# Optimization experiments

Measured on AMD Instinct MI355X. Metric: run time of the kernel, lower is better.

The kernel has to match this reference:

```python
import jax, jax.numpy as jnp
import numpy as np
import math

D_INNER = 1024
D_STATE = 16
DT_RANK = 64  # d_inner // 16


def setup_inputs() -> dict:
    key = jax.random.key(0)
    ks = jax.random.split(key, 8)
    B, L, M, D, R = 2, 2048, D_INNER, D_STATE, DT_RANK
    x = jax.random.normal(ks[0], (B, L, M), dtype=jnp.float32)
    z = jax.random.normal(ks[1], (B, L, M), dtype=jnp.float32)
    # Parameters (torch Linear weight layout: [out, in])
    x_proj_w = jax.random.normal(ks[2], (R + 2 * D, M), dtype=jnp.float32) / jnp.sqrt(M)
    dt_init_std = R ** (-0.5)
    dt_proj_w = jax.random.uniform(ks[3], (M, R), dtype=jnp.float32, minval=-dt_init_std, maxval=dt_init_std)
    dt_min, dt_max = 0.001, 0.1
    dt = jnp.exp(jax.random.uniform(ks[4], (M,), dtype=jnp.float32) * (math.log(dt_max) - math.log(dt_min)) + math.log(dt_min))
    dt_proj_b = dt + jnp.log(-jnp.expm1(-dt))  # inverse softplus init
    A_log = jax.random.normal(ks[5], (D, M), dtype=jnp.float32) * 0.1
    D_param = jnp.ones((M,), dtype=jnp.float32)
    return {"x": x, "z": z, "x_proj_w": x_proj_w, "dt_proj_w": dt_proj_w,
            "dt_proj_b": dt_proj_b, "A_log": A_log, "D_param": D_param}


def reference(x, z, x_proj_w, dt_proj_w, dt_proj_b, A_log, D_param):
    B, L, M = x.shape
    D = A_log.shape[0]
    R = dt_proj_w.shape[1]
    # Input-dependent projections
    xp = jnp.einsum('blm,nm->bln', x, x_proj_w)          # [B,L,R+2D]
    dt_in = xp[..., :R]
    B_ssm = xp[..., R:R + D]                              # [B,L,D]
    C_ssm = xp[..., R + D:]                               # [B,L,D]
    dt = jax.nn.softplus(jnp.einsum('blr,mr->blm', dt_in, dt_proj_w) + dt_proj_b)  # [B,L,M]
    A = -jnp.exp(A_log).T                                 # [M,D]

    def step(h, inp):
        dt_t, x_t, B_t, C_t = inp                         # [B,M],[B,M],[B,D],[B,D]
        dA = jnp.exp(dt_t[:, :, None] * A[None])          # [B,M,D]
        h = dA * h + (dt_t * x_t)[:, :, None] * B_t[:, None, :]
        y_t = jnp.einsum('bmd,bd->bm', h, C_t) + D_param * x_t
        return h, y_t

    h0 = jnp.zeros((B, M, D), dtype=x.dtype)
    xs = (jnp.swapaxes(dt, 0, 1), jnp.swapaxes(x, 0, 1),
          jnp.swapaxes(B_ssm, 0, 1), jnp.swapaxes(C_ssm, 0, 1))
    _, ys = jax.lax.scan(step, h0, xs)                    # ys: [L,B,M]
    y = jnp.swapaxes(ys, 0, 1)
    y = y * jax.nn.silu(z)
    return y
```

## Files before the change

kernel.cpp:

```cpp
#include <hip/hip_runtime.h>
#include <math.h>

#define BB 2
#define LL 2048
#define MM 1024
#define DD 16
#define RR 64
#define NN 96
#define BLROWS (BB*LL)
#define NCH 64
#define CLEN (LL/NCH)

#define OFF_XP    0
#define OFF_DT    (OFF_XP + BLROWS*NN)
#define OFF_A2    (OFF_DT + BLROWS*MM/2)
#define OFF_HEND  (OFF_A2 + MM*DD)
#define OFF_DTSUM (OFF_HEND + NCH*BB*MM*DD)

typedef __attribute__((ext_vector_type(8))) short bf16x8;
typedef __attribute__((ext_vector_type(4))) float f32x4;
typedef __attribute__((ext_vector_type(4))) unsigned short u16x4;

union BF8 { bf16x8 v; unsigned u[4]; };

__device__ __forceinline__ unsigned cvtpk(float a, float b) {
  unsigned r;
  asm("v_cvt_pk_bf16_f32 %0, %1, %2" : "=v"(r) : "v"(a), "v"(b));
  return r;
}

__device__ __forceinline__ float softplusf(float v) {
  return v > 20.f ? v : __logf(1.f + __expf(v));
}

__device__ __forceinline__ short f2bf(float f) {
  union { float f; unsigned u; } v; v.f = f;
  unsigned r = v.u + 0x7FFFu + ((v.u >> 16) & 1u);
  return (short)(r >> 16);
}

__device__ __forceinline__ float bf2f(unsigned short u) {
  return __uint_as_float((unsigned)u << 16);
}

__device__ __forceinline__ float dpp_xor1(float v) {
  int i = __builtin_amdgcn_mov_dpp(__float_as_int(v), 0xB1, 0xF, 0xF, true);
  return __int_as_float(i);
}
__device__ __forceinline__ float dpp_xor2(float v) {
  int i = __builtin_amdgcn_mov_dpp(__float_as_int(v), 0x4E, 0xF, 0xF, true);
  return __int_as_float(i);
}

#define XP_GEMM_BLOCKS ((BLROWS/16)*3)
__global__ __launch_bounds__(64) void k_xp(const float* __restrict__ x,
                                           const float* __restrict__ W,
                                           const float* __restrict__ A_log,
                                           float* __restrict__ ws) {
  if (blockIdx.x >= XP_GEMM_BLOCKS) {
    int idx = (blockIdx.x - XP_GEMM_BLOCKS) * 64 + threadIdx.x;
    int m = idx >> 4, d = idx & 15;
    ws[OFF_A2 + idx] = -__expf(A_log[d * MM + m]);
    return;
  }
  float* xp = ws + OFF_XP;
  int lane = threadIdx.x;
  int rt = blockIdx.x / 3, np = blockIdx.x % 3;
  int lr = lane & 15, lk = lane >> 4;
  const float* xr = x + (size_t)(rt * 16 + lr) * MM + lk * 8;
  const float* wr0 = W + (size_t)(np * 32 + lr) * MM + lk * 8;
  const float* wr1 = W + (size_t)(np * 32 + 16 + lr) * MM + lk * 8;
  f32x4 acc0 = {0.f, 0.f, 0.f, 0.f}, acc1 = {0.f, 0.f, 0.f, 0.f};
#pragma unroll 2
  for (int kk = 0; kk < MM; kk += 32) {
    float4 xa = *(const float4*)(xr + kk);
    float4 xb = *(const float4*)(xr + kk + 4);
    float4 p0 = *(const float4*)(wr0 + kk);
    float4 p1 = *(const float4*)(wr0 + kk + 4);
    float4 q0 = *(const float4*)(wr1 + kk);
    float4 q1 = *(const float4*)(wr1 + kk + 4);
    BF8 a, b0, b1;
    a.u[0] = cvtpk(xa.x, xa.y); a.u[1] = cvtpk(xa.z, xa.w);
    a.u[2] = cvtpk(xb.x, xb.y); a.u[3] = cvtpk(xb.z, xb.w);
    b0.u[0] = cvtpk(p0.x, p0.y); b0.u[1] = cvtpk(p0.z, p0.w);
    b0.u[2] = cvtpk(p1.x, p1.y); b0.u[3] = cvtpk(p1.z, p1.w);
    b1.u[0] = cvtpk(q0.x, q0.y); b1.u[1] = cvtpk(q0.z, q0.w);
    b1.u[2] = cvtpk(q1.x, q1.y); b1.u[3] = cvtpk(q1.z, q1.w);
    acc0 = __builtin_amdgcn_mfma_f32_16x16x32_bf16(a.v, b0.v, acc0, 0, 0, 0);
    acc1 = __builtin_amdgcn_mfma_f32_16x16x32_bf16(a.v, b1.v, acc1, 0, 0, 0);
  }
  int r0 = rt * 16 + lk * 4, c0 = np * 32 + lr;
#pragma unroll
  for (int e = 0; e < 4; ++e) {
    xp[(size_t)(r0 + e) * NN + c0] = acc0[e];
    xp[(size_t)(r0 + e) * NN + c0 + 16] = acc1[e];
  }
}

__global__ __launch_bounds__(64) void k_dt(const float* __restrict__ dtW,
                                           const float* __restrict__ dtb,
                                           float* __restrict__ ws) {
  const float* xp = ws + OFF_XP;
  unsigned short* dt16 = (unsigned short*)(ws + OFF_DT);
  int lane = threadIdx.x;
  int rt = blockIdx.x >> 3, mg = blockIdx.x & 7;
  int lr = lane & 15, lk = lane >> 4;
  const float* xr = xp + (size_t)(rt * 16 + lr) * NN + lk * 8;
  BF8 a0, a1;
  {
    float4 xa = *(const float4*)(xr);
    float4 xb = *(const float4*)(xr + 4);
    float4 xc = *(const float4*)(xr + 32);
    float4 xd = *(const float4*)(xr + 36);
    a0.u[0] = cvtpk(xa.x, xa.y); a0.u[1] = cvtpk(xa.z, xa.w);
    a0.u[2] = cvtpk(xb.x, xb.y); a0.u[3] = cvtpk(xb.z, xb.w);
    a1.u[0] = cvtpk(xc.x, xc.y); a1.u[1] = cvtpk(xc.z, xc.w);
    a1.u[2] = cvtpk(xd.x, xd.y); a1.u[3] = cvtpk(xd.z, xd.w);
  }
  int r0 = rt * 16 + lk * 4;
#pragma unroll 2
  for (int mt = 0; mt < 8; ++mt) {
    int mcol = (mg * 8 + mt) * 16 + lr;
    const float* wr = dtW + (size_t)mcol * RR + lk * 8;
    float4 p0 = *(const float4*)(wr);
    float4 p1 = *(const float4*)(wr + 4);
    float4 p2 = *(const float4*)(wr + 32);
    float4 p3 = *(const float4*)(wr + 36);
    BF8 b0, b1;
    b0.u[0] = cvtpk(p0.x, p0.y); b0.u[1] = cvtpk(p0.z, p0.w);
    b0.u[2] = cvtpk(p1.x, p1.y); b0.u[3] = cvtpk(p1.z, p1.w);
    b1.u[0] = cvtpk(p2.x, p2.y); b1.u[1] = cvtpk(p2.z, p2.w);
    b1.u[2] = cvtpk(p3.x, p3.y); b1.u[3] = cvtpk(p3.z, p3.w);
    f32x4 acc = {0.f, 0.f, 0.f, 0.f};
    acc = __builtin_amdgcn_mfma_f32_16x16x32_bf16(a0.v, b0.v, acc, 0, 0, 0);
    acc = __builtin_amdgcn_mfma_f32_16x16x32_bf16(a1.v, b1.v, acc, 0, 0, 0);
    float bv = dtb[mcol];
#pragma unroll
    for (int e = 0; e < 4; ++e)
      dt16[(size_t)(r0 + e) * MM + mcol] = (unsigned short)f2bf(softplusf(acc[e] + bv));
  }
}

__global__ __launch_bounds__(256) void k_scan1(const float* __restrict__ x,
                                               float* __restrict__ ws) {
  const float* xp = ws + OFF_XP;
  const float* A2t = ws + OFF_A2;
  float* hend = ws + OFF_HEND;
  float* dtsum = ws + OFF_DTSUM;
  __shared__ __align__(16) float ds_[CLEN * 64];
  __shared__ __align__(16) float xs_[CLEN * 64];
  __shared__ __align__(16) float bs[CLEN * DD];
  int wg = blockIdx.x;
  int mw = wg & 15, c = (wg >> 4) & (NCH - 1), b = wg >> 10;
  int t = threadIdx.x;
  int ml = t >> 2, dsub = t & 3;
  int m0 = mw * 64, m = m0 + ml;
  int l0 = c * CLEN;
  const unsigned short* dtg = (const unsigned short*)(ws + OFF_DT) + (size_t)(b * LL + l0) * MM + m0;
  const float* xg = x + (size_t)(b * LL + l0) * MM + m0;
#pragma unroll
  for (int i = t; i < CLEN * 16; i += 256) {
    int lo = i >> 4, q = i & 15;
    u16x4 dv = *(const u16x4*)&dtg[(size_t)lo * MM + q * 4];
    *(float4*)&ds_[lo * 64 + q * 4] = make_float4(bf2f(dv[0]), bf2f(dv[1]), bf2f(dv[2]), bf2f(dv[3]));
    *(float4*)&xs_[lo * 64 + q * 4] = *(const float4*)&xg[(size_t)lo * MM + q * 4];
  }
  for (int i = t; i < CLEN * DD; i += 256) {
    int r = i >> 4, cc = i & 15;
    bs[i] = xp[(size_t)(b * LL + l0 + r) * NN + RR + cc];
  }
  __syncthreads();
  float4 A2v = *(const float4*)&A2t[m * DD + dsub * 4];
  float h0_ = 0.f, h1_ = 0.f, h2_ = 0.f, h3_ = 0.f, S = 0.f;
#pragma unroll 4
  for (int lo = 0; lo < CLEN; ++lo) {
    float dtv = ds_[lo * 64 + ml];
    float xv = xs_[lo * 64 + ml];
    float4 Bv = *(const float4*)&bs[lo * DD + dsub * 4];
    S += dtv;
    float dtx = dtv * xv;
    h0_ = __expf(dtv * A2v.x) * h0_ + dtx * Bv.x;
    h1_ = __expf(dtv * A2v.y) * h1_ + dtx * Bv.y;
    h2_ = __expf(dtv * A2v.z) * h2_ + dtx * Bv.z;
    h3_ = __expf(dtv * A2v.w) * h3_ + dtx * Bv.w;
  }
  size_t o = ((size_t)((c * BB + b) * MM + m)) * DD + dsub * 4;
  *(float4*)&hend[o] = make_float4(h0_, h1_, h2_, h3_);
  if (dsub == 0) dtsum[(c * BB + b) * MM + m] = S;
}

__global__ __launch_bounds__(256) void k_scan2(float* __restrict__ ws) {
  int t = blockIdx.x * 256 + threadIdx.x;
  int d = t & 15, m = (t >> 4) & 1023, b = t >> 14;
  float* hend = ws + OFF_HEND;
  const float* dtsum = ws + OFF_DTSUM;
  float A2 = ws[OFF_A2 + m * DD + d];
  const size_t hstride = (size_t)BB * MM * DD;
  const int sstride = BB * MM;
  size_t o = ((size_t)b * MM + m) * DD + d;
  int si = b * MM + m;
  float h = 0.f;
  float he = hend[o], S = dtsum[si];
  for (int c = 0; c < NCH; ++c) {
    float heN = 0.f, SN = 0.f;
    if (c + 1 < NCH) {
      heN = hend[o + hstride];
      SN = dtsum[si + sstride];
    }
    hend[o] = h;
    h = __expf(A2 * S) * h + he;
    he = heN; S = SN;
    o += hstride; si += sstride;
  }
}

__global__ __launch_bounds__(256) void k_scan3(const float* __restrict__ x,
                                               const float* __restrict__ z,
                                               const float* __restrict__ Dp,
                                               float* __restrict__ out,
                                               float* __restrict__ ws) {
  const float* xp = ws + OFF_XP;
  const float* A2t = ws + OFF_A2;
  const float* h0w = ws + OFF_HEND;
  __shared__ __align__(16) float ds_[CLEN * 64];
  __shared__ __align__(16) float xs_[CLEN * 64];
  __shared__ __align__(16) float zs_[CLEN * 64];
  __shared__ __align__(16) float bs[CLEN * 32];
  int wg = blockIdx.x;
  int mw = wg & 15, c = (wg >> 4) & (NCH - 1), b = wg >> 10;
  int t = threadIdx.x;
  int ml = t >> 2, dsub = t & 3;
  int m0 = mw * 64, m = m0 + ml;
  int l0 = c * CLEN;
  const unsigned short* dtg = (const unsigned short*)(ws + OFF_DT) + (size_t)(b * LL + l0) * MM + m0;
  const float* xg = x + (size_t)(b * LL + l0) * MM + m0;
  const float* zg = z + (size_t)(b * LL + l0) * MM + m0;
#pragma unroll
  for (int i = t; i < CLEN * 16; i += 256) {
    int lo = i >> 4, q = i & 15;
    u16x4 dv = *(const u16x4*)&dtg[(size_t)lo * MM + q * 4];
    *(float4*)&ds_[lo * 64 + q * 4] = make_float4(bf2f(dv[0]), bf2f(dv[1]), bf2f(dv[2]), bf2f(dv[3]));
    *(float4*)&xs_[lo * 64 + q * 4] = *(const float4*)&xg[(size_t)lo * MM + q * 4];
    *(float4*)&zs_[lo * 64 + q * 4] = *(const float4*)&zg[(size_t)lo * MM + q * 4];
  }
  for (int i = t; i < CLEN * 32; i += 256) {
    int r = i >> 5, cc = i & 31;
    bs[i] = xp[(size_t)(b * LL + l0 + r) * NN + RR + cc];
  }
  __syncthreads();
  float4 A2v = *(const float4*)&A2t[m * DD + dsub * 4];
  size_t o = ((size_t)((c * BB + b) * MM + m)) * DD + dsub * 4;
  float4 hv = *(const float4*)&h0w[o];
  float h0_ = hv.x, h1_ = hv.y, h2_ = hv.z, h3_ = hv.w;
  float Dpm = Dp[m];
  size_t idx = ((size_t)(b * LL + l0)) * MM + m;
#pragma unroll 4
  for (int lo = 0; lo < CLEN; ++lo) {
    float dtv = ds_[lo * 64 + ml];
    float xv = xs_[lo * 64 + ml];
    float zv = zs_[lo * 64 + ml];
    float4 Bv = *(const float4*)&bs[lo * 32 + dsub * 4];
    float4 Cv = *(const float4*)&bs[lo * 32 + DD + dsub * 4];
    float dtx = dtv * xv;
    h0_ = __expf(dtv * A2v.x) * h0_ + dtx * Bv.x;
    h1_ = __expf(dtv * A2v.y) * h1_ + dtx * Bv.y;
    h2_ = __expf(dtv * A2v.z) * h2_ + dtx * Bv.z;
    h3_ = __expf(dtv * A2v.w) * h3_ + dtx * Bv.w;
    float yp = h0_ * Cv.x + h1_ * Cv.y + h2_ * Cv.z + h3_ * Cv.w;
    yp += dpp_xor1(yp);
    yp += dpp_xor2(yp);
    float sig = __builtin_amdgcn_rcpf(1.f + __expf(-zv));
    if (dsub == 0)
      out[idx + (size_t)lo * MM] = (yp + Dpm * xv) * zv * sig;
  }
}

extern "C" void kernel_launch(void* const* d_in, const int* in_sizes, int n_in,
                              void* d_out, int out_size, void* d_ws, size_t ws_size,
                              hipStream_t stream) {
  const float* x = (const float*)d_in[0];
  const float* z = (const float*)d_in[1];
  const float* W = (const float*)d_in[2];
  const float* dtW = (const float*)d_in[3];
  const float* dtb = (const float*)d_in[4];
  const float* A_log = (const float*)d_in[5];
  const float* Dp = (const float*)d_in[6];
  float* out = (float*)d_out;
  float* ws = (float*)d_ws;

  k_xp<<<XP_GEMM_BLOCKS + (MM * DD / 64), 64, 0, stream>>>(x, W, A_log, ws);
  k_dt<<<(BLROWS / 16) * 8, 64, 0, stream>>>(dtW, dtb, ws);
  k_scan1<<<16 * NCH * BB, 256, 0, stream>>>(x, ws);
  k_scan2<<<128, 256, 0, stream>>>(ws);
  k_scan3<<<16 * NCH * BB, 256, 0, stream>>>(x, z, Dp, out, ws);
}
```

Measured before the change: 85.96 us.

## Split-K xp GEMM across four waves, widen dt grid, store scan inputs as bf16 in LDS

The x-projection GEMM now uses 256-thread blocks in which each wave handles a quarter of K, and the partial sums are reduced through shared memory, so four times as many waves work on each output tile. The dt projection grid is doubled, with each block covering four M-tiles instead of eight. The scan kernels keep dt, x and z in LDS as bf16 rather than fp32, and dt is copied with a single 16-byte load per thread. This halves LDS footprint, which may raise occupancy, at the cost of bf16 rounding of x and z in the recurrence and output, which could reduce accuracy.

```diff
diff --git a/kernel.cpp b/kernel.cpp
--- a/kernel.cpp
+++ b/kernel.cpp
@@ -19,7 +19,6 @@
 
 typedef __attribute__((ext_vector_type(8))) short bf16x8;
 typedef __attribute__((ext_vector_type(4))) float f32x4;
-typedef __attribute__((ext_vector_type(4))) unsigned short u16x4;
 
 union BF8 { bf16x8 v; unsigned u[4]; };
 
@@ -53,26 +52,28 @@
 }
 
 #define XP_GEMM_BLOCKS ((BLROWS/16)*3)
-__global__ __launch_bounds__(64) void k_xp(const float* __restrict__ x,
-                                           const float* __restrict__ W,
-                                           const float* __restrict__ A_log,
-                                           float* __restrict__ ws) {
+__global__ __launch_bounds__(256) void k_xp(const float* __restrict__ x,
+                                            const float* __restrict__ W,
+                                            const float* __restrict__ A_log,
+                                            float* __restrict__ ws) {
   if (blockIdx.x >= XP_GEMM_BLOCKS) {
-    int idx = (blockIdx.x - XP_GEMM_BLOCKS) * 64 + threadIdx.x;
-    int m = idx >> 4, d = idx & 15;
-    ws[OFF_A2 + idx] = -__expf(A_log[d * MM + m]);
+    int idx = (blockIdx.x - XP_GEMM_BLOCKS) * 256 + threadIdx.x;
+    if (idx < MM * DD) {
+      int m = idx >> 4, d = idx & 15;
+      ws[OFF_A2 + idx] = -__expf(A_log[d * MM + m]);
+    }
     return;
   }
-  float* xp = ws + OFF_XP;
-  int lane = threadIdx.x;
+  __shared__ __align__(16) float red[4][8][68];
+  int t = threadIdx.x, w = t >> 6, lane = t & 63;
   int rt = blockIdx.x / 3, np = blockIdx.x % 3;
   int lr = lane & 15, lk = lane >> 4;
-  const float* xr = x + (size_t)(rt * 16 + lr) * MM + lk * 8;
-  const float* wr0 = W + (size_t)(np * 32 + lr) * MM + lk * 8;
-  const float* wr1 = W + (size_t)(np * 32 + 16 + lr) * MM + lk * 8;
+  const float* xr = x + (size_t)(rt * 16 + lr) * MM + w * 256 + lk * 8;
+  const float* wr0 = W + (size_t)(np * 32 + lr) * MM + w * 256 + lk * 8;
+  const float* wr1 = W + (size_t)(np * 32 + 16 + lr) * MM + w * 256 + lk * 8;
   f32x4 acc0 = {0.f, 0.f, 0.f, 0.f}, acc1 = {0.f, 0.f, 0.f, 0.f};
 #pragma unroll 2
-  for (int kk = 0; kk < MM; kk += 32) {
+  for (int kk = 0; kk < 256; kk += 32) {
     float4 xa = *(const float4*)(xr + kk);
     float4 xb = *(const float4*)(xr + kk + 4);
     float4 p0 = *(const float4*)(wr0 + kk);
@@ -89,11 +90,20 @@
     acc0 = __builtin_amdgcn_mfma_f32_16x16x32_bf16(a.v, b0.v, acc0, 0, 0, 0);
     acc1 = __builtin_amdgcn_mfma_f32_16x16x32_bf16(a.v, b1.v, acc1, 0, 0, 0);
   }
-  int r0 = rt * 16 + lk * 4, c0 = np * 32 + lr;
 #pragma unroll
   for (int e = 0; e < 4; ++e) {
-    xp[(size_t)(r0 + e) * NN + c0] = acc0[e];
-    xp[(size_t)(r0 + e) * NN + c0 + 16] = acc1[e];
+    red[w][e][lane] = acc0[e];
+    red[w][4 + e][lane] = acc1[e];
+  }
+  __syncthreads();
+  float* xp = ws + OFF_XP;
+#pragma unroll
+  for (int v = t; v < 512; v += 256) {
+    int row = v >> 5, col = v & 31;
+    int ln = ((row >> 2) << 4) | (col & 15);
+    int sub = ((col >> 4) << 2) | (row & 3);
+    float s = red[0][sub][ln] + red[1][sub][ln] + red[2][sub][ln] + red[3][sub][ln];
+    xp[(size_t)(rt * 16 + row) * NN + np * 32 + col] = s;
   }
 }
 
@@ -103,7 +113,7 @@
   const float* xp = ws + OFF_XP;
   unsigned short* dt16 = (unsigned short*)(ws + OFF_DT);
   int lane = threadIdx.x;
-  int rt = blockIdx.x >> 3, mg = blockIdx.x & 7;
+  int rt = blockIdx.x >> 4, mg = blockIdx.x & 15;
   int lr = lane & 15, lk = lane >> 4;
   const float* xr = xp + (size_t)(rt * 16 + lr) * NN + lk * 8;
   BF8 a0, a1;
@@ -119,8 +129,8 @@
   }
   int r0 = rt * 16 + lk * 4;
 #pragma unroll 2
-  for (int mt = 0; mt < 8; ++mt) {
-    int mcol = (mg * 8 + mt) * 16 + lr;
+  for (int mt = 0; mt < 4; ++mt) {
+    int mcol = (mg * 4 + mt) * 16 + lr;
     const float* wr = dtW + (size_t)mcol * RR + lk * 8;
     float4 p0 = *(const float4*)(wr);
     float4 p1 = *(const float4*)(wr + 4);
@@ -147,8 +157,8 @@
   const float* A2t = ws + OFF_A2;
   float* hend = ws + OFF_HEND;
   float* dtsum = ws + OFF_DTSUM;
-  __shared__ __align__(16) float ds_[CLEN * 64];
-  __shared__ __align__(16) float xs_[CLEN * 64];
+  __shared__ __align__(16) unsigned short ds16[CLEN * 64];
+  __shared__ __align__(16) unsigned short xs16[CLEN * 64];
   __shared__ __align__(16) float bs[CLEN * DD];
   int wg = blockIdx.x;
   int mw = wg & 15, c = (wg >> 4) & (NCH - 1), b = wg >> 10;
@@ -158,13 +168,18 @@
   int l0 = c * CLEN;
   const unsigned short* dtg = (const unsigned short*)(ws + OFF_DT) + (size_t)(b * LL + l0) * MM + m0;
   const float* xg = x + (size_t)(b * LL + l0) * MM + m0;
+  {
+    int lo = t >> 3, g = t & 7;
+    *(uint4*)&ds16[lo * 64 + g * 8] = *(const uint4*)&dtg[(size_t)lo * MM + g * 8];
+  }
 #pragma unroll
   for (int i = t; i < CLEN * 16; i += 256) {
     int lo = i >> 4, q = i & 15;
-    u16x4 dv = *(const u16x4*)&dtg[(size_t)lo * MM + q * 4];
-    *(float4*)&ds_[lo * 64 + q * 4] = make_float4(bf2f(dv[0]), bf2f(dv[1]), bf2f(dv[2]), bf2f(dv[3]));
-    *(float4*)&xs_[lo * 64 + q * 4] = *(const float4*)&xg[(size_t)lo * MM + q * 4];
-  }
+    float4 xv = *(const float4*)&xg[(size_t)lo * MM + q * 4];
+    uint2 xpk; xpk.x = cvtpk(xv.x, xv.y); xpk.y = cvtpk(xv.z, xv.w);
+    *(uint2*)&xs16[lo * 64 + q * 4] = xpk;
+  }
+#pragma unroll
   for (int i = t; i < CLEN * DD; i += 256) {
     int r = i >> 4, cc = i & 15;
     bs[i] = xp[(size_t)(b * LL + l0 + r) * NN + RR + cc];
@@ -174,8 +189,8 @@
   float h0_ = 0.f, h1_ = 0.f, h2_ = 0.f, h3_ = 0.f, S = 0.f;
 #pragma unroll 4
   for (int lo = 0; lo < CLEN; ++lo) {
-    float dtv = ds_[lo * 64 + ml];
-    float xv = xs_[lo * 64 + ml];
+    float dtv = bf2f(ds16[lo * 64 + ml]);
+    float xv = bf2f(xs16[lo * 64 + ml]);
     float4 Bv = *(const float4*)&bs[lo * DD + dsub * 4];
     S += dtv;
     float dtx = dtv * xv;
@@ -222,9 +237,9 @@
   const float* xp = ws + OFF_XP;
   const float* A2t = ws + OFF_A2;
   const float* h0w = ws + OFF_HEND;
-  __shared__ __align__(16) float ds_[CLEN * 64];
-  __shared__ __align__(16) float xs_[CLEN * 64];
-  __shared__ __align__(16) float zs_[CLEN * 64];
+  __shared__ __align__(16) unsigned short ds16[CLEN * 64];
+  __shared__ __align__(16) unsigned short xs16[CLEN * 64];
+  __shared__ __align__(16) unsigned short zs16[CLEN * 64];
   __shared__ __align__(16) float bs[CLEN * 32];
   int wg = blockIdx.x;
   int mw = wg & 15, c = (wg >> 4) & (NCH - 1), b = wg >> 10;
@@ -235,14 +250,21 @@
   const unsigned short* dtg = (const unsigned short*)(ws + OFF_DT) + (size_t)(b * LL + l0) * MM + m0;
   const float* xg = x + (size_t)(b * LL + l0) * MM + m0;
   const float* zg = z + (size_t)(b * LL + l0) * MM + m0;
+  {
+    int lo = t >> 3, g = t & 7;
+    *(uint4*)&ds16[lo * 64 + g * 8] = *(const uint4*)&dtg[(size_t)lo * MM + g * 8];
+  }
 #pragma unroll
   for (int i = t; i < CLEN * 16; i += 256) {
     int lo = i >> 4, q = i & 15;
-    u16x4 dv = *(const u16x4*)&dtg[(size_t)lo * MM + q * 4];
-    *(float4*)&ds_[lo * 64 + q * 4] = make_float4(bf2f(dv[0]), bf2f(dv[1]), bf2f(dv[2]), bf2f(dv[3]));
-    *(float4*)&xs_[lo * 64 + q * 4] = *(const float4*)&xg[(size_t)lo * MM + q * 4];
-    *(float4*)&zs_[lo * 64 + q * 4] = *(const float4*)&zg[(size_t)lo * MM + q * 4];
-  }
+    float4 xv = *(const float4*)&xg[(size_t)lo * MM + q * 4];
+    float4 zv = *(const float4*)&zg[(size_t)lo * MM + q * 4];
+    uint2 xpk; xpk.x = cvtpk(xv.x, xv.y); xpk.y = cvtpk(xv.z, xv.w);
+    uint2 zpk; zpk.x = cvtpk(zv.x, zv.y); zpk.y = cvtpk(zv.z, zv.w);
+    *(uint2*)&xs16[lo * 64 + q * 4] = xpk;
+    *(uint2*)&zs16[lo * 64 + q * 4] = zpk;
+  }
+#pragma unroll
   for (int i = t; i < CLEN * 32; i += 256) {
     int r = i >> 5, cc = i & 31;
     bs[i] = xp[(size_t)(b * LL + l0 + r) * NN + RR + cc];
@@ -256,9 +278,9 @@
   size_t idx = ((size_t)(b * LL + l0)) * MM + m;
 #pragma unroll 4
   for (int lo = 0; lo < CLEN; ++lo) {
-    float dtv = ds_[lo * 64 + ml];
-    float xv = xs_[lo * 64 + ml];
-    float zv = zs_[lo * 64 + ml];
+    float dtv = bf2f(ds16[lo * 64 + ml]);
+    float xv = bf2f(xs16[lo * 64 + ml]);
+    float zv = bf2f(zs16[lo * 64 + ml]);
     float4 Bv = *(const float4*)&bs[lo * 32 + dsub * 4];
     float4 Cv = *(const float4*)&bs[lo * 32 + DD + dsub * 4];
     float dtx = dtv * xv;
@@ -288,8 +310,8 @@
   float* out = (float*)d_out;
   float* ws = (float*)d_ws;
 
-  k_xp<<<XP_GEMM_BLOCKS + (MM * DD / 64), 64, 0, stream>>>(x, W, A_log, ws);
-  k_dt<<<(BLROWS / 16) * 8, 64, 0, stream>>>(dtW, dtb, ws);
+  k_xp<<<XP_GEMM_BLOCKS + (MM * DD / 256), 256, 0, stream>>>(x, W, A_log, ws);
+  k_dt<<<(BLROWS / 16) * 16, 64, 0, stream>>>(dtW, dtb, ws);
   k_scan1<<<16 * NCH * BB, 256, 0, stream>>>(x, ws);
   k_scan2<<<128, 256, 0, stream>>>(ws);
   k_scan3<<<16 * NCH * BB, 256, 0, stream>>>(x, z, Dp, out, ws);
```

Result: slower. 90.67 us (+5.5%).
